# Optimization experiments

Measured on AMD Instinct MI355X. Metric: run time of the kernel, lower is better.

Reference implementation:

```python
import jax, jax.numpy as jnp
import numpy as np


def _layernorm(x, g, b, eps=1e-5):
    mu = x.mean(-1, keepdims=True)
    var = ((x - mu) ** 2).mean(-1, keepdims=True)
    return (x - mu) / jnp.sqrt(var + eps) * g + b


def setup_inputs() -> dict:
    B, I, J, M, H = 2, 8, 1025, 256, 8
    Dh = M // H
    key = jax.random.key(0)
    ks = jax.random.split(key, 8)
    bound1 = 1.0 / np.sqrt(M)      # nn.Linear(M, 4M) init bound
    bound2 = 1.0 / np.sqrt(4 * M)  # nn.Linear(4M, M) init bound
    return {
        "x": jnp.zeros((B, J - 1, 1, I), dtype=jnp.int32),  # shape-carrier only
        "savespace": jax.random.normal(ks[0], (B, I, J, M), dtype=jnp.float32),
        "Wqkv": jax.random.normal(ks[1], (3, H, Dh, M), dtype=jnp.float32),
        "Wo": jax.random.normal(ks[2], (M, M), dtype=jnp.float32),
        "ln1_g": jnp.ones((M,), jnp.float32),
        "ln1_b": jnp.zeros((M,), jnp.float32),
        "ln2_g": jnp.ones((M,), jnp.float32),
        "ln2_b": jnp.zeros((M,), jnp.float32),
        "fc1_w": jax.random.uniform(ks[3], (4 * M, M), jnp.float32, -bound1, bound1),
        "fc1_b": jax.random.uniform(ks[4], (4 * M,), jnp.float32, -bound1, bound1),
        "fc2_w": jax.random.uniform(ks[5], (M, 4 * M), jnp.float32, -bound2, bound2),
        "fc2_b": jax.random.uniform(ks[6], (M,), jnp.float32, -bound2, bound2),
    }


def reference(x, savespace, Wqkv, Wo, ln1_g, ln1_b, ln2_g, ln2_b, fc1_w, fc1_b, fc2_w, fc2_b):
    # savespace: [B, I, J, M]
    B, I, J, M = savespace.shape
    Dh = Wqkv.shape[2]
    scale = 1.0 / (Dh ** 0.5)

    s_ln = _layernorm(savespace, ln1_g, ln1_b)
    # 'xhdm,bijm->bxijhd' followed by transpose(2,3): produce [B, I, H, J, Dh] directly
    q = jnp.einsum('hdm,bijm->bihjd', Wqkv[0], s_ln)
    k = jnp.einsum('hdm,bijm->bihjd', Wqkv[1], s_ln)
    v = jnp.einsum('hdm,bijm->bihjd', Wqkv[2], s_ln)

    # unnormalized attention: NO softmax in the original module
    scores = jnp.einsum('bihjd,bihkd->bihjk', q * scale, k)  # [B, I, H, J, J]
    imv = jnp.einsum('bihjk,bihkd->bijhd', scores, v)         # [B, I, J, H, Dh]
    imv = imv.reshape(B, I, J, M)

    # FAITHFUL to buggy einsum 'nm,bijn->bijn': elementwise scale by Wo row-sums
    s2 = Wo.sum(axis=1) * imv + savespace

    h = _layernorm(s2, ln2_g, ln2_b)
    h = jax.nn.gelu(h @ fc1_w.T + fc1_b, approximate=False)  # torch nn.GELU = exact erf
    h = h @ fc2_w.T + fc2_b
    return h + s2
```

## Files before the change

### kernel.cpp

```cpp
#include <hip/hip_runtime.h>
#include <hip/hip_bf16.h>
#include <math.h>

#define BB   2
#define II   8
#define JJ   1025
#define MM   256
#define HH   8
#define DH   32
#define BI   (BB*II)
#define RTOT (BI*JJ)
#define NQKV (3*MM)
#define HID  (4*MM)
#define MPAD 16512

#define BM 64
#define BN 128
#define BK 32
#define LP 40

#define S2P 260

#define WQN (NQKV*MM)
#define W1N (HID*MM)
#define W2N (MM*HID)

typedef unsigned short ushort;
typedef __attribute__((ext_vector_type(8))) short short8;
typedef __attribute__((ext_vector_type(4))) float f32x4;
typedef __attribute__((ext_vector_type(4))) ushort ushort4v;

__device__ __forceinline__ ushort f2bf(float x) {
    __hip_bfloat16 h = __float2bfloat16(x);
    return *reinterpret_cast<ushort*>(&h);
}
__device__ __forceinline__ float bf2f(ushort u) {
    __hip_bfloat16 h = *reinterpret_cast<__hip_bfloat16*>(&u);
    return __bfloat162float(h);
}
__device__ __forceinline__ float gelu_exact(float x) {
    return 0.5f * x * (1.0f + erff(x * 0.70710678118654752f));
}
__device__ __forceinline__ float wave_sum(float v) {
#pragma unroll
    for (int off = 32; off > 0; off >>= 1) v += __shfl_xor(v, off);
    return v;
}
__device__ __forceinline__ float block_sum256(float v, float* red, int t) {
    red[t] = v; __syncthreads();
    for (int s = 128; s > 0; s >>= 1) {
        if (t < s) red[t] += red[t + s];
        __syncthreads();
    }
    float r = red[0]; __syncthreads();
    return r;
}

__global__ __launch_bounds__(256) void k_prep(
    const float* __restrict__ wq, const float* __restrict__ w1,
    const float* __restrict__ w2, const float* __restrict__ Wo,
    const float* __restrict__ save, const float* __restrict__ g1,
    const float* __restrict__ b1,
    ushort* __restrict__ dq, ushort* __restrict__ d1, ushort* __restrict__ d2,
    float* __restrict__ woSum, float* __restrict__ KtV,
    ushort* __restrict__ Ah)
{
    __shared__ float red[256];
    const int gb = blockIdx.x, t = threadIdx.x;
    if (gb < 768) {
        int i = gb * 256 + t;
        dq[i] = f2bf(wq[i]);
    } else if (gb < 832) {
        int u = (gb - 768) * 256 + t;
        int lane = u & 63, frag = u >> 6;
        int kf = frag & 7, nt = frag >> 3;
        int n = nt * 16 + (lane & 15);
        int k = kf * 32 + (lane >> 4) * 8;
        const float* src = w1 + (size_t)n * MM + k;
        ushort4v o0, o1;
#pragma unroll
        for (int c = 0; c < 4; ++c) { o0[c] = f2bf(src[c]); o1[c] = f2bf(src[4 + c]); }
        *(ushort4v*)&d1[(size_t)u * 8]     = o0;
        *(ushort4v*)&d1[(size_t)u * 8 + 4] = o1;
    } else if (gb < 896) {
        int u = (gb - 832) * 256 + t;
        int lane = u & 63, frag = u >> 6;
        int kh = frag & 15, nt2 = frag >> 4;
        int n = nt2 * 16 + (lane & 15);
        int k = kh * 32 + (lane >> 4) * 8;
        const float* src = w2 + (size_t)n * HID + k;
        ushort4v o0, o1;
#pragma unroll
        for (int c = 0; c < 4; ++c) { o0[c] = f2bf(src[c]); o1[c] = f2bf(src[4 + c]); }
        *(ushort4v*)&d2[(size_t)u * 8]     = o0;
        *(ushort4v*)&d2[(size_t)u * 8 + 4] = o1;
    } else if (gb < 1152) {
        int m = gb - 896;
        float s = block_sum256(Wo[m * MM + t], red, t);
        if (t == 0) woSum[m] = s;
    } else if (gb < 1664) {
        KtV[(gb - 1152) * 256 + t] = 0.0f;
    } else {
        const int wave = t >> 6, l = t & 63;
        const int row = (gb - 1664) * 4 + wave;
        const size_t base = (size_t)row * MM + 4 * l;
        if (row >= RTOT) { ushort4v z = 0; *(ushort4v*)&Ah[base] = z; return; }
        f32x4 v = *(const f32x4*)&save[base];
        float mu = wave_sum(v[0] + v[1] + v[2] + v[3]) * (1.0f / MM);
        f32x4 d;
#pragma unroll
        for (int c = 0; c < 4; ++c) d[c] = v[c] - mu;
        float var = wave_sum(d[0]*d[0] + d[1]*d[1] + d[2]*d[2] + d[3]*d[3]) * (1.0f / MM);
        float rstd = 1.0f / sqrtf(var + 1e-5f);
        f32x4 g = *(const f32x4*)&g1[4 * l];
        f32x4 b = *(const f32x4*)&b1[4 * l];
        ushort4v o;
#pragma unroll
        for (int c = 0; c < 4; ++c) o[c] = f2bf(d[c] * rstd * g[c] + b[c]);
        *(ushort4v*)&Ah[base] = o;
    }
}

__global__ __launch_bounds__(256, 4) void k_qkv_gemm(
    const ushort* __restrict__ A, const ushort* __restrict__ W,
    ushort* __restrict__ Cout)
{
    __shared__ __align__(16) ushort sA[2][BM * LP];
    __shared__ __align__(16) ushort sB[2][BN * LP];

    const int tid  = threadIdx.x;
    const int wave = tid >> 6;
    const int lane = tid & 63;
    const int lrow = lane & 15;
    const int quad = lane >> 4;
    const int row0 = blockIdx.y * BM;
    const int col0 = blockIdx.x * BN;
    const int ar = tid >> 2;
    const int ac = (tid & 3) * 8;
    const int K = MM, KT = MM / BK;

    f32x4 acc[4][2] = {};

    f32x4 ra, rb0, rb1;
    ra  = *(const f32x4*)(A + (size_t)(row0 + ar) * K + ac);
    rb0 = *(const f32x4*)(W + (size_t)(col0 + ar) * K + ac);
    rb1 = *(const f32x4*)(W + (size_t)(col0 + ar + 64) * K + ac);
    *(f32x4*)&sA[0][ar * LP + ac] = ra;
    *(f32x4*)&sB[0][ar * LP + ac] = rb0;
    *(f32x4*)&sB[0][(ar + 64) * LP + ac] = rb1;

    for (int kt = 0; kt < KT; ++kt) {
        __syncthreads();
        const int cur = kt & 1, nxt = cur ^ 1;
        const bool more = (kt + 1 < KT);
        if (more) {
            const int kk = (kt + 1) * BK;
            ra  = *(const f32x4*)(A + (size_t)(row0 + ar) * K + kk + ac);
            rb0 = *(const f32x4*)(W + (size_t)(col0 + ar) * K + kk + ac);
            rb1 = *(const f32x4*)(W + (size_t)(col0 + ar + 64) * K + kk + ac);
        }
        short8 fa[4], fb[2];
#pragma unroll
        for (int i = 0; i < 4; ++i)
            fa[i] = *(const short8*)&sA[cur][(i * 16 + lrow) * LP + quad * 8];
#pragma unroll
        for (int j = 0; j < 2; ++j)
            fb[j] = *(const short8*)&sB[cur][(wave * 32 + j * 16 + lrow) * LP + quad * 8];
#pragma unroll
        for (int i = 0; i < 4; ++i)
#pragma unroll
            for (int j = 0; j < 2; ++j)
                acc[i][j] = __builtin_amdgcn_mfma_f32_16x16x32_bf16(
                    fa[i], fb[j], acc[i][j], 0, 0, 0);
        if (more) {
            *(f32x4*)&sA[nxt][ar * LP + ac] = ra;
            *(f32x4*)&sB[nxt][ar * LP + ac] = rb0;
            *(f32x4*)&sB[nxt][(ar + 64) * LP + ac] = rb1;
        }
    }
#pragma unroll
    for (int i = 0; i < 4; ++i)
#pragma unroll
        for (int j = 0; j < 2; ++j) {
            const int ncol = col0 + wave * 32 + j * 16 + lrow;
#pragma unroll
            for (int v = 0; v < 4; ++v) {
                const int r = row0 + i * 16 + quad * 4 + v;
                Cout[(size_t)r * NQKV + ncol] = f2bf(acc[i][j][v]);
            }
        }
}

__global__ __launch_bounds__(256) void k_ktv(const ushort* __restrict__ qkv,
                                             float* __restrict__ KtV) {
    __shared__ float Ks[8][32];
    __shared__ float Vs[8][32];

    const int bih = blockIdx.x;
    const int sp  = blockIdx.y;
    const int bi = bih >> 3;
    const int h  = bih & 7;
    const ushort* baseK = qkv + (size_t)bi * JJ * NQKV + MM     + h * DH;
    const ushort* baseV = qkv + (size_t)bi * JJ * NQKV + 2 * MM + h * DH;

    const int jbeg = sp * 129;
    const int jend = min(JJ, jbeg + 129);

    const int t = threadIdx.x;
    const int srow = t >> 5;
    const int scol = t & 31;
    const int d2 = t & 31;
    const int d1b = t >> 5;

    float acc[4] = {0.f, 0.f, 0.f, 0.f};

    for (int jb = jbeg; jb < jend; jb += 8) {
        int j = jb + srow;
        float kv = 0.f, vv = 0.f;
        if (j < jend) {
            kv = bf2f(baseK[(size_t)j * NQKV + scol]);
            vv = bf2f(baseV[(size_t)j * NQKV + scol]);
        }
        Ks[srow][scol] = kv;
        Vs[srow][scol] = vv;
        __syncthreads();
#pragma unroll
        for (int jl = 0; jl < 8; ++jl) {
            float v = Vs[jl][d2];
#pragma unroll
            for (int p = 0; p < 4; ++p) acc[p] += Ks[jl][d1b + 8 * p] * v;
        }
        __syncthreads();
    }

    const float scale = 0.17677669529663687f;
    float* out = KtV + (size_t)bih * 1024;
#pragma unroll
    for (int p = 0; p < 4; ++p)
        atomicAdd(&out[(d1b + 8 * p) * DH + d2], scale * acc[p]);
}

__global__ __launch_bounds__(256) void k_ktvb(const float* __restrict__ KtV,
                                              ushort* __restrict__ KtVB) {
    const int bi = blockIdx.x, t = threadIdx.x;
#pragma unroll
    for (int rep = 0; rep < 4; ++rep) {
        const int slot = rep * 256 + t;
        const int lane = slot & 63;
        const int nt   = (slot >> 6) & 1;
        const int h    = slot >> 7;
        const int d2   = nt * 16 + (lane & 15);
        const int d1b  = (lane >> 4) * 8;
        const float* src = KtV + ((size_t)(bi * 8 + h)) * 1024 + d2;
        ushort4v o0, o1;
#pragma unroll
        for (int i = 0; i < 4; ++i) {
            o0[i] = f2bf(src[(size_t)(d1b + i) * 32]);
            o1[i] = f2bf(src[(size_t)(d1b + 4 + i) * 32]);
        }
        ushort* dst = KtVB + (size_t)bi * 8192 + (size_t)slot * 8;
        *(ushort4v*)dst       = o0;
        *(ushort4v*)(dst + 4) = o1;
    }
}

__global__ __launch_bounds__(256, 4) void k_imv_mlp(
    const ushort* __restrict__ qkv, const ushort* __restrict__ KtVB,
    const float* __restrict__ woSum, const float* __restrict__ save,
    const float* __restrict__ g2, const float* __restrict__ b2,
    const ushort* __restrict__ F1B, const ushort* __restrict__ F2B,
    const float* __restrict__ fb1, const float* __restrict__ fb2,
    float* __restrict__ out)
{
    __shared__ __align__(16) ushort sA[16 * 264];
    __shared__ __align__(16) ushort sH[2][16 * 72];
    __shared__ __align__(16) float  s2t[16 * S2P];

    const int tid = threadIdx.x, wave = tid >> 6, l = tid & 63;
    const int lrow = l & 15, quad = l >> 4;
    const int bi = blockIdx.x / 65;
    const int jb = (blockIdx.x % 65) * 16;

    const ushort* kb = KtVB + (size_t)bi * 8192 + (size_t)(wave * 2) * 1024 + (size_t)l * 8;
    short8 kf0 = *(const short8*)(kb);
    short8 kf1 = *(const short8*)(kb + 512);
    short8 kf2h = *(const short8*)(kb + 1024);
    short8 kf3 = *(const short8*)(kb + 1536);

    const ushort* f1base = F1B + (size_t)(wave * 8) * 512 + (size_t)l * 8;
    const ushort* f2base = F2B + (size_t)(wave * 64) * 512 + (size_t)l * 8;
    short8 wf1[8];
#pragma unroll
    for (int kf = 0; kf < 8; ++kf)
        wf1[kf] = *(const short8*)(f1base + (size_t)kf * 512);

#pragma unroll
    for (int it = 0; it < 2; ++it) {
        int lin = it * 256 + tid;
        int r = lin >> 5, c = (lin & 31) * 8;
        int j = jb + r;
        f32x4 qv = {};
        if (j < JJ) qv = *(const f32x4*)&qkv[((size_t)(bi * JJ + j)) * NQKV + c];
        *(f32x4*)&sA[r * 264 + c] = qv;
    }
    __syncthreads();

    f32x4 c4[4];
    {
        short8 a0 = *(const short8*)&sA[lrow * 264 + (wave * 2 + 0) * 32 + quad * 8];
        short8 a1 = *(const short8*)&sA[lrow * 264 + (wave * 2 + 1) * 32 + quad * 8];
        f32x4 z = {};
        c4[0] = __builtin_amdgcn_mfma_f32_16x16x32_bf16(a0, kf0, z, 0, 0, 0);
        c4[1] = __builtin_amdgcn_mfma_f32_16x16x32_bf16(a0, kf1, z, 0, 0, 0);
        c4[2] = __builtin_amdgcn_mfma_f32_16x16x32_bf16(a1, kf2h, z, 0, 0, 0);
        c4[3] = __builtin_amdgcn_mfma_f32_16x16x32_bf16(a1, kf3, z, 0, 0, 0);
    }
#pragma unroll
    for (int f = 0; f < 4; ++f) {
        const int col = (wave * 2 + (f >> 1)) * 32 + (f & 1) * 16 + lrow;
#pragma unroll
        for (int v = 0; v < 4; ++v)
            s2t[(quad * 4 + v) * S2P + col] = c4[f][v];
    }
    __syncthreads();

    {
        f32x4 ws = *(const f32x4*)&woSum[4 * l];
        f32x4 g  = *(const f32x4*)&g2[4 * l];
        f32x4 b  = *(const f32x4*)&b2[4 * l];
#pragma unroll
        for (int rr = 0; rr < 4; ++rr) {
            const int lr = wave * 4 + rr;
            const int j  = jb + lr;
            const bool valid = (j < JJ);
            const size_t base = ((size_t)(bi * JJ + (valid ? j : 0))) * MM + 4 * l;
            f32x4 imv4 = *(const f32x4*)&s2t[lr * S2P + 4 * l];
            f32x4 sv = {};
            if (valid) sv = *(const f32x4*)&save[base];
            f32x4 val;
#pragma unroll
            for (int c = 0; c < 4; ++c) val[c] = ws[c] * imv4[c] + sv[c];
            float mu = wave_sum(val[0] + val[1] + val[2] + val[3]) * (1.0f / MM);
            f32x4 d;
#pragma unroll
            for (int c = 0; c < 4; ++c) d[c] = val[c] - mu;
            float var = wave_sum(d[0]*d[0] + d[1]*d[1] + d[2]*d[2] + d[3]*d[3]) * (1.0f / MM);
            float rstd = 1.0f / sqrtf(var + 1e-5f);
            *(f32x4*)&s2t[lr * S2P + 4 * l] = val;
            ushort4v o;
#pragma unroll
            for (int c = 0; c < 4; ++c) o[c] = f2bf(d[c] * rstd * g[c] + b[c]);
            *(ushort4v*)&sA[lr * 264 + 4 * l] = o;
        }
    }

    float bv1[8];
#pragma unroll
    for (int cc = 0; cc < 8; ++cc) bv1[cc] = fb1[cc * 64 + wave * 16 + lrow];

    __syncthreads();

    f32x4 acc2[4] = {};

#pragma unroll
    for (int cc = 0; cc < 8; ++cc) {
        short8 wf1n[8];
        if (cc < 7) {
#pragma unroll
            for (int kf = 0; kf < 8; ++kf)
                wf1n[kf] = *(const short8*)(f1base + (size_t)((cc + 1) * 32 + kf) * 512);
        }
        short8 wf2[8];
#pragma unroll
        for (int jt = 0; jt < 4; ++jt)
#pragma unroll
            for (int k2 = 0; k2 < 2; ++k2)
                wf2[jt * 2 + k2] = *(const short8*)(
                    f2base + (size_t)(jt * 16 + cc * 2 + k2) * 512);

        f32x4 acc1 = {};
#pragma unroll
        for (int kf = 0; kf < 8; ++kf) {
            short8 fa0 = *(const short8*)&sA[lrow * 264 + kf * 32 + quad * 8];
            acc1 = __builtin_amdgcn_mfma_f32_16x16x32_bf16(fa0, wf1[kf], acc1, 0, 0, 0);
        }
#pragma unroll
        for (int v = 0; v < 4; ++v) {
            float hv = gelu_exact(acc1[v] + bv1[cc]);
            sH[cc & 1][(quad * 4 + v) * 72 + wave * 16 + lrow] = f2bf(hv);
        }
        __syncthreads();
#pragma unroll
        for (int k2 = 0; k2 < 2; ++k2) {
            short8 ha0 = *(const short8*)&sH[cc & 1][lrow * 72 + k2 * 32 + quad * 8];
#pragma unroll
            for (int jt = 0; jt < 4; ++jt)
                acc2[jt] = __builtin_amdgcn_mfma_f32_16x16x32_bf16(ha0, wf2[jt * 2 + k2], acc2[jt], 0, 0, 0);
        }
        if (cc < 7) {
#pragma unroll
            for (int kf = 0; kf < 8; ++kf) wf1[kf] = wf1n[kf];
        }
    }

#pragma unroll
    for (int jt = 0; jt < 4; ++jt) {
        const int col = wave * 64 + jt * 16 + lrow;
        const float bv = fb2[col];
#pragma unroll
        for (int v = 0; v < 4; ++v) {
            const int lr = quad * 4 + v;
            const int j  = jb + lr;
            if (j < JJ)
                out[((size_t)(bi * JJ + j)) * MM + col] =
                    acc2[jt][v] + bv + s2t[lr * S2P + col];
        }
    }
}

extern "C" void kernel_launch(void* const* d_in, const int* in_sizes, int n_in,
                              void* d_out, int out_size, void* d_ws, size_t ws_size,
                              hipStream_t stream) {
    const float* savespace = (const float*)d_in[1];
    const float* Wqkv      = (const float*)d_in[2];
    const float* Wo        = (const float*)d_in[3];
    const float* ln1_g     = (const float*)d_in[4];
    const float* ln1_b     = (const float*)d_in[5];
    const float* ln2_g     = (const float*)d_in[6];
    const float* ln2_b     = (const float*)d_in[7];
    const float* fc1_w     = (const float*)d_in[8];
    const float* fc1_b     = (const float*)d_in[9];
    const float* fc2_w     = (const float*)d_in[10];
    const float* fc2_b     = (const float*)d_in[11];
    float* out = (float*)d_out;

    char* w = (char*)d_ws;
    ushort* Ah    = (ushort*)w;
    ushort* qkv   = (ushort*)(w + 8454144);
    char* c4 = w + 8454144 + 25362432;
    ushort* WqkvB = (ushort*)c4;
    ushort* F1B   = (ushort*)(c4 + WQN * 2);
    ushort* F2B   = (ushort*)(c4 + WQN * 2 + W1N * 2);
    float*  KtV   = (float*) (c4 + WQN * 2 + W1N * 2 + W2N * 2);
    float*  woSum = (float*) (c4 + WQN * 2 + W1N * 2 + W2N * 2 + 524288);
    ushort* KtVB  = (ushort*)(c4 + WQN * 2 + W1N * 2 + W2N * 2 + 524288 + 4096);

    k_prep<<<1664 + MPAD / 4, 256, 0, stream>>>(
        Wqkv, fc1_w, fc2_w, Wo, savespace, ln1_g, ln1_b,
        WqkvB, F1B, F2B, woSum, KtV, Ah);
    {
        dim3 grid(NQKV / BN, MPAD / BM);
        k_qkv_gemm<<<grid, 256, 0, stream>>>(Ah, WqkvB, qkv);
    }
    {
        dim3 grid(BI * HH, 8);
        k_ktv<<<grid, 256, 0, stream>>>(qkv, KtV);
    }
    k_ktvb<<<BI, 256, 0, stream>>>(KtV, KtVB);
    k_imv_mlp<<<BI * 65, 256, 0, stream>>>(qkv, KtVB, woSum, savespace,
                                           ln2_g, ln2_b, F1B, F2B,
                                           fc1_b, fc2_b, out);
}
```

Baseline: 168.3 us.

## Process 32 rows per block in fused imv+MLP kernel to reuse weight fragments

Each block of the fused imv/LN2/MLP kernel now handles 32 token rows in two 16-row subtiles instead of 16. The fc1/fc2 weight fragments loaded from global memory are reused across both subtiles, halving weight traffic per row, and the grid shrinks from 1040 to 528 blocks. The cost is more LDS and registers (launch bounds lowered to 2 blocks per CU), an extra barrier per subtile, and fewer blocks to spread across the CUs.

```diff
diff --git a/kernel.cpp b/kernel.cpp
--- a/kernel.cpp
+++ b/kernel.cpp
@@ -264,7 +264,7 @@
     }
 }
 
-__global__ __launch_bounds__(256, 4) void k_imv_mlp(
+__global__ __launch_bounds__(256, 2) void k_imv_mlp(
     const ushort* __restrict__ qkv, const ushort* __restrict__ KtVB,
     const float* __restrict__ woSum, const float* __restrict__ save,
     const float* __restrict__ g2, const float* __restrict__ b2,
@@ -272,20 +272,21 @@
     const float* __restrict__ fb1, const float* __restrict__ fb2,
     float* __restrict__ out)
 {
-    __shared__ __align__(16) ushort sA[16 * 264];
+    __shared__ __align__(16) ushort sA[32 * 264];
+    __shared__ __align__(16) float  s2f[32 * S2P];
     __shared__ __align__(16) ushort sH[2][16 * 72];
-    __shared__ __align__(16) float  s2t[16 * S2P];
+    __shared__ __align__(16) ushort sQ[16 * 264];
 
     const int tid = threadIdx.x, wave = tid >> 6, l = tid & 63;
     const int lrow = l & 15, quad = l >> 4;
-    const int bi = blockIdx.x / 65;
-    const int jb = (blockIdx.x % 65) * 16;
+    const int bi = blockIdx.x / 33;
+    const int jb = (blockIdx.x % 33) * 32;
 
     const ushort* kb = KtVB + (size_t)bi * 8192 + (size_t)(wave * 2) * 1024 + (size_t)l * 8;
-    short8 kf0 = *(const short8*)(kb);
-    short8 kf1 = *(const short8*)(kb + 512);
-    short8 kf2h = *(const short8*)(kb + 1024);
-    short8 kf3 = *(const short8*)(kb + 1536);
+    const short8 kf0 = *(const short8*)(kb);
+    const short8 kf1 = *(const short8*)(kb + 512);
+    const short8 kf2h = *(const short8*)(kb + 1024);
+    const short8 kf3 = *(const short8*)(kb + 1536);
 
     const ushort* f1base = F1B + (size_t)(wave * 8) * 512 + (size_t)l * 8;
     const ushort* f2base = F2B + (size_t)(wave * 64) * 512 + (size_t)l * 8;
@@ -294,47 +295,49 @@
     for (int kf = 0; kf < 8; ++kf)
         wf1[kf] = *(const short8*)(f1base + (size_t)kf * 512);
 
-#pragma unroll
-    for (int it = 0; it < 2; ++it) {
-        int lin = it * 256 + tid;
-        int r = lin >> 5, c = (lin & 31) * 8;
-        int j = jb + r;
-        f32x4 qv = {};
-        if (j < JJ) qv = *(const f32x4*)&qkv[((size_t)(bi * JJ + j)) * NQKV + c];
-        *(f32x4*)&sA[r * 264 + c] = qv;
-    }
-    __syncthreads();
-
-    f32x4 c4[4];
-    {
-        short8 a0 = *(const short8*)&sA[lrow * 264 + (wave * 2 + 0) * 32 + quad * 8];
-        short8 a1 = *(const short8*)&sA[lrow * 264 + (wave * 2 + 1) * 32 + quad * 8];
-        f32x4 z = {};
-        c4[0] = __builtin_amdgcn_mfma_f32_16x16x32_bf16(a0, kf0, z, 0, 0, 0);
-        c4[1] = __builtin_amdgcn_mfma_f32_16x16x32_bf16(a0, kf1, z, 0, 0, 0);
-        c4[2] = __builtin_amdgcn_mfma_f32_16x16x32_bf16(a1, kf2h, z, 0, 0, 0);
-        c4[3] = __builtin_amdgcn_mfma_f32_16x16x32_bf16(a1, kf3, z, 0, 0, 0);
-    }
-#pragma unroll
-    for (int f = 0; f < 4; ++f) {
-        const int col = (wave * 2 + (f >> 1)) * 32 + (f & 1) * 16 + lrow;
-#pragma unroll
-        for (int v = 0; v < 4; ++v)
-            s2t[(quad * 4 + v) * S2P + col] = c4[f][v];
-    }
-    __syncthreads();
-
-    {
-        f32x4 ws = *(const f32x4*)&woSum[4 * l];
-        f32x4 g  = *(const f32x4*)&g2[4 * l];
-        f32x4 b  = *(const f32x4*)&b2[4 * l];
+    const f32x4 ws = *(const f32x4*)&woSum[4 * l];
+    const f32x4 g  = *(const f32x4*)&g2[4 * l];
+    const f32x4 b  = *(const f32x4*)&b2[4 * l];
+
+#pragma unroll
+    for (int rt = 0; rt < 2; ++rt) {
+#pragma unroll
+        for (int it = 0; it < 2; ++it) {
+            int lin = it * 256 + tid;
+            int r = lin >> 5, c = (lin & 31) * 8;
+            int j = jb + rt * 16 + r;
+            f32x4 qv = {};
+            if (j < JJ) qv = *(const f32x4*)&qkv[((size_t)(bi * JJ + j)) * NQKV + c];
+            *(f32x4*)&sQ[r * 264 + c] = qv;
+        }
+        __syncthreads();
+
+        f32x4 c4[4];
+        {
+            short8 a0 = *(const short8*)&sQ[lrow * 264 + (wave * 2 + 0) * 32 + quad * 8];
+            short8 a1 = *(const short8*)&sQ[lrow * 264 + (wave * 2 + 1) * 32 + quad * 8];
+            f32x4 z = {};
+            c4[0] = __builtin_amdgcn_mfma_f32_16x16x32_bf16(a0, kf0, z, 0, 0, 0);
+            c4[1] = __builtin_amdgcn_mfma_f32_16x16x32_bf16(a0, kf1, z, 0, 0, 0);
+            c4[2] = __builtin_amdgcn_mfma_f32_16x16x32_bf16(a1, kf2h, z, 0, 0, 0);
+            c4[3] = __builtin_amdgcn_mfma_f32_16x16x32_bf16(a1, kf3, z, 0, 0, 0);
+        }
+#pragma unroll
+        for (int f = 0; f < 4; ++f) {
+            const int col = (wave * 2 + (f >> 1)) * 32 + (f & 1) * 16 + lrow;
+#pragma unroll
+            for (int v = 0; v < 4; ++v)
+                s2f[(rt * 16 + quad * 4 + v) * S2P + col] = c4[f][v];
+        }
+        __syncthreads();
+
 #pragma unroll
         for (int rr = 0; rr < 4; ++rr) {
-            const int lr = wave * 4 + rr;
+            const int lr = rt * 16 + wave * 4 + rr;
             const int j  = jb + lr;
             const bool valid = (j < JJ);
             const size_t base = ((size_t)(bi * JJ + (valid ? j : 0))) * MM + 4 * l;
-            f32x4 imv4 = *(const f32x4*)&s2t[lr * S2P + 4 * l];
+            f32x4 imv4 = *(const f32x4*)&s2f[lr * S2P + 4 * l];
             f32x4 sv = {};
             if (valid) sv = *(const f32x4*)&save[base];
             f32x4 val;
@@ -346,21 +349,20 @@
             for (int c = 0; c < 4; ++c) d[c] = val[c] - mu;
             float var = wave_sum(d[0]*d[0] + d[1]*d[1] + d[2]*d[2] + d[3]*d[3]) * (1.0f / MM);
             float rstd = 1.0f / sqrtf(var + 1e-5f);
-            *(f32x4*)&s2t[lr * S2P + 4 * l] = val;
+            *(f32x4*)&s2f[lr * S2P + 4 * l] = val;
             ushort4v o;
 #pragma unroll
             for (int c = 0; c < 4; ++c) o[c] = f2bf(d[c] * rstd * g[c] + b[c]);
             *(ushort4v*)&sA[lr * 264 + 4 * l] = o;
         }
+        __syncthreads();
     }
 
     float bv1[8];
 #pragma unroll
     for (int cc = 0; cc < 8; ++cc) bv1[cc] = fb1[cc * 64 + wave * 16 + lrow];
 
-    __syncthreads();
-
-    f32x4 acc2[4] = {};
+    f32x4 acc2[2][4] = {};
 
 #pragma unroll
     for (int cc = 0; cc < 8; ++cc) {
@@ -378,24 +380,29 @@
                 wf2[jt * 2 + k2] = *(const short8*)(
                     f2base + (size_t)(jt * 16 + cc * 2 + k2) * 512);
 
-        f32x4 acc1 = {};
-#pragma unroll
-        for (int kf = 0; kf < 8; ++kf) {
-            short8 fa0 = *(const short8*)&sA[lrow * 264 + kf * 32 + quad * 8];
-            acc1 = __builtin_amdgcn_mfma_f32_16x16x32_bf16(fa0, wf1[kf], acc1, 0, 0, 0);
-        }
-#pragma unroll
-        for (int v = 0; v < 4; ++v) {
-            float hv = gelu_exact(acc1[v] + bv1[cc]);
-            sH[cc & 1][(quad * 4 + v) * 72 + wave * 16 + lrow] = f2bf(hv);
-        }
-        __syncthreads();
-#pragma unroll
-        for (int k2 = 0; k2 < 2; ++k2) {
-            short8 ha0 = *(const short8*)&sH[cc & 1][lrow * 72 + k2 * 32 + quad * 8];
-#pragma unroll
-            for (int jt = 0; jt < 4; ++jt)
-                acc2[jt] = __builtin_amdgcn_mfma_f32_16x16x32_bf16(ha0, wf2[jt * 2 + k2], acc2[jt], 0, 0, 0);
+#pragma unroll
+        for (int rt = 0; rt < 2; ++rt) {
+            const int sb = (cc * 2 + rt) & 1;
+            f32x4 acc1 = {};
+#pragma unroll
+            for (int kf = 0; kf < 8; ++kf) {
+                short8 fa0 = *(const short8*)&sA[(rt * 16 + lrow) * 264 + kf * 32 + quad * 8];
+                acc1 = __builtin_amdgcn_mfma_f32_16x16x32_bf16(fa0, wf1[kf], acc1, 0, 0, 0);
+            }
+#pragma unroll
+            for (int v = 0; v < 4; ++v) {
+                float hv = gelu_exact(acc1[v] + bv1[cc]);
+                sH[sb][(quad * 4 + v) * 72 + wave * 16 + lrow] = f2bf(hv);
+            }
+            __syncthreads();
+#pragma unroll
+            for (int k2 = 0; k2 < 2; ++k2) {
+                short8 ha0 = *(const short8*)&sH[sb][lrow * 72 + k2 * 32 + quad * 8];
+#pragma unroll
+                for (int jt = 0; jt < 4; ++jt)
+                    acc2[rt][jt] = __builtin_amdgcn_mfma_f32_16x16x32_bf16(
+                        ha0, wf2[jt * 2 + k2], acc2[rt][jt], 0, 0, 0);
+            }
         }
         if (cc < 7) {
 #pragma unroll
@@ -408,13 +415,15 @@
         const int col = wave * 64 + jt * 16 + lrow;
         const float bv = fb2[col];
 #pragma unroll
-        for (int v = 0; v < 4; ++v) {
-            const int lr = quad * 4 + v;
-            const int j  = jb + lr;
-            if (j < JJ)
-                out[((size_t)(bi * JJ + j)) * MM + col] =
-                    acc2[jt][v] + bv + s2t[lr * S2P + col];
-        }
+        for (int rt = 0; rt < 2; ++rt)
+#pragma unroll
+            for (int v = 0; v < 4; ++v) {
+                const int lr = rt * 16 + quad * 4 + v;
+                const int j  = jb + lr;
+                if (j < JJ)
+                    out[((size_t)(bi * JJ + j)) * MM + col] =
+                        acc2[rt][jt][v] + bv + s2f[lr * S2P + col];
+            }
     }
 }
 
@@ -457,7 +466,7 @@
         k_ktv<<<grid, 256, 0, stream>>>(qkv, KtV);
     }
     k_ktvb<<<BI, 256, 0, stream>>>(KtV, KtVB);
-    k_imv_mlp<<<BI * 65, 256, 0, stream>>>(qkv, KtVB, woSum, savespace,
+    k_imv_mlp<<<BI * 33, 256, 0, stream>>>(qkv, KtVB, woSum, savespace,
                                            ln2_g, ln2_b, F1B, F2B,
                                            fc1_b, fc2_b, out);
 }
```

Result: slower. 180.1 us (+7.0%).

## Fuse LayerNorm1 into the QKV GEMM and slim the prep kernel

Applied to the files above, without the earlier changes.

LayerNorm of savespace moves out of the prep kernel and into the QKV GEMM. Each block normalizes its 64 rows straight into a full-K LDS A tile, so the bf16 Ah intermediate is never written to or read from global memory. The prep kernel also gets vectorized weight conversion, a wave-level Wo row sum and vectorized KtV zeroing, which cuts its block count. In exchange, each GEMM block recomputes LayerNorm for its rows once per column block (six times in total) and reads fp32 savespace repeatedly. The larger LDS tile also lowers occupancy, with launch bounds going from 4 to 3.

```diff
diff --git a/kernel.cpp b/kernel.cpp
--- a/kernel.cpp
+++ b/kernel.cpp
@@ -17,7 +17,8 @@
 #define BM 64
 #define BN 128
 #define BK 32
-#define LP 40
+#define APITCH 264
+#define BPITCH 40
 
 #define S2P 260
 
@@ -46,32 +47,23 @@
     for (int off = 32; off > 0; off >>= 1) v += __shfl_xor(v, off);
     return v;
 }
-__device__ __forceinline__ float block_sum256(float v, float* red, int t) {
-    red[t] = v; __syncthreads();
-    for (int s = 128; s > 0; s >>= 1) {
-        if (t < s) red[t] += red[t + s];
-        __syncthreads();
-    }
-    float r = red[0]; __syncthreads();
-    return r;
-}
 
 __global__ __launch_bounds__(256) void k_prep(
     const float* __restrict__ wq, const float* __restrict__ w1,
     const float* __restrict__ w2, const float* __restrict__ Wo,
-    const float* __restrict__ save, const float* __restrict__ g1,
-    const float* __restrict__ b1,
     ushort* __restrict__ dq, ushort* __restrict__ d1, ushort* __restrict__ d2,
-    float* __restrict__ woSum, float* __restrict__ KtV,
-    ushort* __restrict__ Ah)
+    float* __restrict__ woSum, float* __restrict__ KtV)
 {
-    __shared__ float red[256];
     const int gb = blockIdx.x, t = threadIdx.x;
-    if (gb < 768) {
-        int i = gb * 256 + t;
-        dq[i] = f2bf(wq[i]);
-    } else if (gb < 832) {
-        int u = (gb - 768) * 256 + t;
+    if (gb < 192) {
+        int i = (gb * 256 + t) * 4;
+        f32x4 v = *(const f32x4*)&wq[i];
+        ushort4v o;
+#pragma unroll
+        for (int c = 0; c < 4; ++c) o[c] = f2bf(v[c]);
+        *(ushort4v*)&dq[i] = o;
+    } else if (gb < 256) {
+        int u = (gb - 192) * 256 + t;
         int lane = u & 63, frag = u >> 6;
         int kf = frag & 7, nt = frag >> 3;
         int n = nt * 16 + (lane & 15);
@@ -82,8 +74,8 @@
         for (int c = 0; c < 4; ++c) { o0[c] = f2bf(src[c]); o1[c] = f2bf(src[4 + c]); }
         *(ushort4v*)&d1[(size_t)u * 8]     = o0;
         *(ushort4v*)&d1[(size_t)u * 8 + 4] = o1;
-    } else if (gb < 896) {
-        int u = (gb - 832) * 256 + t;
+    } else if (gb < 320) {
+        int u = (gb - 256) * 256 + t;
         int lane = u & 63, frag = u >> 6;
         int kh = frag & 15, nt2 = frag >> 4;
         int n = nt2 * 16 + (lane & 15);
@@ -94,39 +86,27 @@
         for (int c = 0; c < 4; ++c) { o0[c] = f2bf(src[c]); o1[c] = f2bf(src[4 + c]); }
         *(ushort4v*)&d2[(size_t)u * 8]     = o0;
         *(ushort4v*)&d2[(size_t)u * 8 + 4] = o1;
-    } else if (gb < 1152) {
-        int m = gb - 896;
-        float s = block_sum256(Wo[m * MM + t], red, t);
-        if (t == 0) woSum[m] = s;
-    } else if (gb < 1664) {
-        KtV[(gb - 1152) * 256 + t] = 0.0f;
+    } else if (gb < 384) {
+        const int wave = t >> 6, l = t & 63;
+        const int m = (gb - 320) * 4 + wave;
+        float s = Wo[m * MM + l] + Wo[m * MM + 64 + l]
+                + Wo[m * MM + 128 + l] + Wo[m * MM + 192 + l];
+        s = wave_sum(s);
+        if (l == 0) woSum[m] = s;
     } else {
-        const int wave = t >> 6, l = t & 63;
-        const int row = (gb - 1664) * 4 + wave;
-        const size_t base = (size_t)row * MM + 4 * l;
-        if (row >= RTOT) { ushort4v z = 0; *(ushort4v*)&Ah[base] = z; return; }
-        f32x4 v = *(const f32x4*)&save[base];
-        float mu = wave_sum(v[0] + v[1] + v[2] + v[3]) * (1.0f / MM);
-        f32x4 d;
-#pragma unroll
-        for (int c = 0; c < 4; ++c) d[c] = v[c] - mu;
-        float var = wave_sum(d[0]*d[0] + d[1]*d[1] + d[2]*d[2] + d[3]*d[3]) * (1.0f / MM);
-        float rstd = 1.0f / sqrtf(var + 1e-5f);
-        f32x4 g = *(const f32x4*)&g1[4 * l];
-        f32x4 b = *(const f32x4*)&b1[4 * l];
-        ushort4v o;
-#pragma unroll
-        for (int c = 0; c < 4; ++c) o[c] = f2bf(d[c] * rstd * g[c] + b[c]);
-        *(ushort4v*)&Ah[base] = o;
-    }
-}
-
-__global__ __launch_bounds__(256, 4) void k_qkv_gemm(
-    const ushort* __restrict__ A, const ushort* __restrict__ W,
+        int idx = (gb - 384) * 256 + t;
+        f32x4 z = {};
+        *(f32x4*)&KtV[(size_t)idx * 4] = z;
+    }
+}
+
+__global__ __launch_bounds__(256, 3) void k_ln_qkv(
+    const float* __restrict__ save, const float* __restrict__ g1,
+    const float* __restrict__ b1, const ushort* __restrict__ W,
     ushort* __restrict__ Cout)
 {
-    __shared__ __align__(16) ushort sA[2][BM * LP];
-    __shared__ __align__(16) ushort sB[2][BN * LP];
+    __shared__ __align__(16) ushort sA[BM * APITCH];
+    __shared__ __align__(16) ushort sB[2][BN * BPITCH];
 
     const int tid  = threadIdx.x;
     const int wave = tid >> 6;
@@ -135,37 +115,57 @@
     const int quad = lane >> 4;
     const int row0 = blockIdx.y * BM;
     const int col0 = blockIdx.x * BN;
+
     const int ar = tid >> 2;
     const int ac = (tid & 3) * 8;
-    const int K = MM, KT = MM / BK;
+    const ushort* wrow0 = W + (size_t)(col0 + ar) * MM + ac;
+    const ushort* wrow1 = W + (size_t)(col0 + ar + 64) * MM + ac;
+
+    f32x4 rb0 = *(const f32x4*)(wrow0);
+    f32x4 rb1 = *(const f32x4*)(wrow1);
+    *(f32x4*)&sB[0][ar * BPITCH + ac] = rb0;
+    *(f32x4*)&sB[0][(ar + 64) * BPITCH + ac] = rb1;
+
+    {
+        const f32x4 g = *(const f32x4*)&g1[4 * lane];
+        const f32x4 b = *(const f32x4*)&b1[4 * lane];
+        for (int rr = 0; rr < 16; ++rr) {
+            const int row = wave * 16 + rr;
+            const int gr  = row0 + row;
+            ushort4v o = 0;
+            if (gr < RTOT) {
+                f32x4 v = *(const f32x4*)&save[(size_t)gr * MM + 4 * lane];
+                float mu = wave_sum(v[0] + v[1] + v[2] + v[3]) * (1.0f / MM);
+                f32x4 d;
+#pragma unroll
+                for (int c = 0; c < 4; ++c) d[c] = v[c] - mu;
+                float var = wave_sum(d[0]*d[0] + d[1]*d[1] + d[2]*d[2] + d[3]*d[3]) * (1.0f / MM);
+                float rstd = 1.0f / sqrtf(var + 1e-5f);
+#pragma unroll
+                for (int c = 0; c < 4; ++c) o[c] = f2bf(d[c] * rstd * g[c] + b[c]);
+            }
+            *(ushort4v*)&sA[row * APITCH + 4 * lane] = o;
+        }
+    }
 
     f32x4 acc[4][2] = {};
 
-    f32x4 ra, rb0, rb1;
-    ra  = *(const f32x4*)(A + (size_t)(row0 + ar) * K + ac);
-    rb0 = *(const f32x4*)(W + (size_t)(col0 + ar) * K + ac);
-    rb1 = *(const f32x4*)(W + (size_t)(col0 + ar + 64) * K + ac);
-    *(f32x4*)&sA[0][ar * LP + ac] = ra;
-    *(f32x4*)&sB[0][ar * LP + ac] = rb0;
-    *(f32x4*)&sB[0][(ar + 64) * LP + ac] = rb1;
-
-    for (int kt = 0; kt < KT; ++kt) {
+    for (int kt = 0; kt < 8; ++kt) {
         __syncthreads();
         const int cur = kt & 1, nxt = cur ^ 1;
-        const bool more = (kt + 1 < KT);
+        const bool more = (kt < 7);
         if (more) {
-            const int kk = (kt + 1) * BK;
-            ra  = *(const f32x4*)(A + (size_t)(row0 + ar) * K + kk + ac);
-            rb0 = *(const f32x4*)(W + (size_t)(col0 + ar) * K + kk + ac);
-            rb1 = *(const f32x4*)(W + (size_t)(col0 + ar + 64) * K + kk + ac);
-        }
+            rb0 = *(const f32x4*)(wrow0 + (kt + 1) * BK);
+            rb1 = *(const f32x4*)(wrow1 + (kt + 1) * BK);
+        }
+
         short8 fa[4], fb[2];
 #pragma unroll
         for (int i = 0; i < 4; ++i)
-            fa[i] = *(const short8*)&sA[cur][(i * 16 + lrow) * LP + quad * 8];
+            fa[i] = *(const short8*)&sA[(i * 16 + lrow) * APITCH + kt * BK + quad * 8];
 #pragma unroll
         for (int j = 0; j < 2; ++j)
-            fb[j] = *(const short8*)&sB[cur][(wave * 32 + j * 16 + lrow) * LP + quad * 8];
+            fb[j] = *(const short8*)&sB[cur][(wave * 32 + j * 16 + lrow) * BPITCH + quad * 8];
 #pragma unroll
         for (int i = 0; i < 4; ++i)
 #pragma unroll
@@ -173,11 +173,11 @@
                 acc[i][j] = __builtin_amdgcn_mfma_f32_16x16x32_bf16(
                     fa[i], fb[j], acc[i][j], 0, 0, 0);
         if (more) {
-            *(f32x4*)&sA[nxt][ar * LP + ac] = ra;
-            *(f32x4*)&sB[nxt][ar * LP + ac] = rb0;
-            *(f32x4*)&sB[nxt][(ar + 64) * LP + ac] = rb1;
-        }
-    }
+            *(f32x4*)&sB[nxt][ar * BPITCH + ac] = rb0;
+            *(f32x4*)&sB[nxt][(ar + 64) * BPITCH + ac] = rb1;
+        }
+    }
+
 #pragma unroll
     for (int i = 0; i < 4; ++i)
 #pragma unroll
@@ -435,9 +435,8 @@
     float* out = (float*)d_out;
 
     char* w = (char*)d_ws;
-    ushort* Ah    = (ushort*)w;
-    ushort* qkv   = (ushort*)(w + 8454144);
-    char* c4 = w + 8454144 + 25362432;
+    ushort* qkv   = (ushort*)w;
+    char* c4 = w + 25362432;
     ushort* WqkvB = (ushort*)c4;
     ushort* F1B   = (ushort*)(c4 + WQN * 2);
     ushort* F2B   = (ushort*)(c4 + WQN * 2 + W1N * 2);
@@ -445,12 +444,11 @@
     float*  woSum = (float*) (c4 + WQN * 2 + W1N * 2 + W2N * 2 + 524288);
     ushort* KtVB  = (ushort*)(c4 + WQN * 2 + W1N * 2 + W2N * 2 + 524288 + 4096);
 
-    k_prep<<<1664 + MPAD / 4, 256, 0, stream>>>(
-        Wqkv, fc1_w, fc2_w, Wo, savespace, ln1_g, ln1_b,
-        WqkvB, F1B, F2B, woSum, KtV, Ah);
+    k_prep<<<512, 256, 0, stream>>>(
+        Wqkv, fc1_w, fc2_w, Wo, WqkvB, F1B, F2B, woSum, KtV);
     {
         dim3 grid(NQKV / BN, MPAD / BM);
-        k_qkv_gemm<<<grid, 256, 0, stream>>>(Ah, WqkvB, qkv);
+        k_ln_qkv<<<grid, 256, 0, stream>>>(savespace, ln1_g, ln1_b, WqkvB, qkv);
     }
     {
         dim3 grid(BI * HH, 8);
```

Measured after the change: 209.6 us. 24.5% more time.
